# Kernel tuning notes

Measured on AMD Instinct MI355X. Metric: run time of the kernel, lower is better.

The kernel has to match this reference:

```python
import jax, jax.numpy as jnp
import numpy as np

H = 512  # hidden_size


def setup_inputs() -> dict:
    key = jax.random.key(0)
    k1, k2, k3, k4, k5 = jax.random.split(key, 5)
    B, S = 32, 2048
    hidden = jax.random.normal(k1, (1, B, H), dtype=jnp.float32)
    encoder_outputs = jax.random.normal(k2, (B, S, 2 * H), dtype=jnp.float32)
    # nn.Linear(3H, H): weight [H, 3H], store transposed [3H, H] for x @ W
    scale_a = 1.0 / np.sqrt(3 * H)
    Wa = jax.random.uniform(k3, (3 * H, H), jnp.float32, -scale_a, scale_a)
    ba = jax.random.uniform(k4, (H,), jnp.float32, -scale_a, scale_a)
    # nn.Linear(H, 1, bias=False): weight [1, H] -> store as [H]
    scale_v = 1.0 / np.sqrt(H)
    v = jax.random.uniform(k5, (H,), jnp.float32, -scale_v, scale_v)
    return {"hidden": hidden, "encoder_outputs": encoder_outputs,
            "Wa": Wa, "ba": ba, "v": v}


def reference(hidden, encoder_outputs, Wa, ba, v):
    # hidden: [1, B, H] -> [B, H]; encoder_outputs: [B, S, 2H]
    h = jnp.squeeze(hidden, axis=0)                      # [B, H]
    # Split concat-linear into two projections (same math as cat + matmul):
    Wh, We = Wa[:H], Wa[H:]                              # [H, H], [2H, H]
    # energy: [B, S, H] = tanh(h Wh + enc We + b), h broadcast over S
    energy = jnp.tanh(h @ Wh + jnp.einsum('bse,eh->bsh', encoder_outputs, We)[..., :, :] + ba) if False else \
             jnp.tanh((h @ Wh)[:, None, :] + jnp.einsum('bse,eh->bsh', encoder_outputs, We) + ba)
    scores = jnp.einsum('bsh,h->bs', energy, v)          # [B, S]
    attention_weights = jax.nn.softmax(scores, axis=1)   # [B, S]
    context = jnp.einsum('bs,bse->be', attention_weights, encoder_outputs)  # [B, 2H]
    return context, attention_weights
```

## Files before the change

kernel.cpp:

```cpp
#include <hip/hip_runtime.h>

typedef unsigned short ushort_t;
typedef __attribute__((ext_vector_type(8))) short bf16x8;
typedef __attribute__((ext_vector_type(4))) float f32x4;

#define H 512
#define E 1024
#define S 2048
#define B 32

__device__ __forceinline__ ushort_t f2bf(float f) {
    unsigned u = __float_as_uint(f);
    unsigned r = (u + 0x7FFFu + ((u >> 16) & 1u)) >> 16;
    return (ushort_t)r;
}

__device__ __forceinline__ uint4 pack8(float4 x, float4 y) {
    uint4 u;
    u.x = (unsigned)f2bf(x.x) | ((unsigned)f2bf(x.y) << 16);
    u.y = (unsigned)f2bf(x.z) | ((unsigned)f2bf(x.w) << 16);
    u.z = (unsigned)f2bf(y.x) | ((unsigned)f2bf(y.y) << 16);
    u.w = (unsigned)f2bf(y.z) | ((unsigned)f2bf(y.w) << 16);
    return u;
}

__global__ void prep_hb(const float* __restrict__ hidden, const float* __restrict__ Wa,
                        const float* __restrict__ ba, float* __restrict__ hb) {
    int b = blockIdx.x, kc = blockIdx.y, tid = threadIdx.x;
    const float* hp = hidden + b * H + kc * 64;
    float a0 = 0.f, a1 = 0.f;
    #pragma unroll 8
    for (int k = 0; k < 64; ++k) {
        float hv = hp[k];
        a0 += hv * Wa[(size_t)(kc * 64 + k) * H + tid];
        a1 += hv * Wa[(size_t)(kc * 64 + k) * H + tid + 256];
    }
    if (kc == 0) { a0 += ba[tid]; a1 += ba[tid + 256]; }
    atomicAdd(&hb[b * H + tid], a0);
    atomicAdd(&hb[b * H + tid + 256], a1);
}

__global__ void prep_wef(const float* __restrict__ Wa, ushort_t* __restrict__ wef) {
    int g = blockIdx.x * 256 + threadIdx.x;
    int kt = g >> 11, nt = (g >> 6) & 31, l = g & 63;
    int kbase = kt * 32 + ((l >> 4) << 3);
    int n = nt * 16 + (l & 15);
    #pragma unroll
    for (int j = 0; j < 8; ++j)
        wef[(size_t)g * 8 + j] = f2bf(Wa[(size_t)(H + kbase + j) * H + n]);
}

__launch_bounds__(256, 2)
__global__ void score_kernel(const float* __restrict__ enc, const ushort_t* __restrict__ wef,
                             const float* __restrict__ hb, const float* __restrict__ v,
                             float* __restrict__ scores) {
    int b = blockIdx.y;
    int s0 = blockIdx.x * 64;
    int tid = threadIdx.x;
    int wave = tid >> 6, lane = tid & 63;
    int q = lane >> 4, nl = lane & 15;

    __shared__ ushort_t Bs[2][32 * 64 * 8];
    __shared__ ushort_t As[2][64 * 40];
    __shared__ float sred[4][64];

    f32x4 acc[4][8] = {};

    int arow = tid >> 2, acol = (tid & 3) * 8;
    const float* asrc = enc + ((size_t)b * S + s0 + arow) * E + acol;

    const ushort_t* bsrc = wef + (size_t)wave * 4096 + (size_t)lane * 8;

    float4 areg[2][2];
    areg[0][0] = *(const float4*)(asrc);
    areg[0][1] = *(const float4*)(asrc + 4);
    areg[1][0] = *(const float4*)(asrc + 32);
    areg[1][1] = *(const float4*)(asrc + 36);

    #pragma unroll
    for (int j = 0; j < 8; ++j)
        __builtin_amdgcn_global_load_lds(
            (const __attribute__((address_space(1))) unsigned*)(bsrc + j * 512),
            (__attribute__((address_space(3))) unsigned*)(&Bs[0][wave * 4096 + j * 512]),
            16, 0, 0);

    *(uint4*)&As[0][arow * 40 + acol] = pack8(areg[0][0], areg[0][1]);
    __syncthreads();

    for (int kt = 0; kt < 32; ++kt) {
        int cur = kt & 1;
        ushort_t* Ac = &As[cur][0];
        ushort_t* Bc = &Bs[cur][0];

        if (kt < 31) {
            const ushort_t* bs = bsrc + (size_t)(kt + 1) * 16384;
            #pragma unroll
            for (int j = 0; j < 8; ++j)
                __builtin_amdgcn_global_load_lds(
                    (const __attribute__((address_space(1))) unsigned*)(bs + j * 512),
                    (__attribute__((address_space(3))) unsigned*)(&Bs[1 - cur][wave * 4096 + j * 512]),
                    16, 0, 0);
            *(uint4*)&As[1 - cur][arow * 40 + acol] =
                pack8(areg[1 - cur][0], areg[1 - cur][1]);
        }
        if (kt < 30) {
            areg[cur][0] = *(const float4*)(asrc + (size_t)(kt + 2) * 32);
            areg[cur][1] = *(const float4*)(asrc + (size_t)(kt + 2) * 32 + 4);
        }

        bf16x8 afr[4];
        #pragma unroll
        for (int mt = 0; mt < 4; ++mt)
            afr[mt] = *(const bf16x8*)&Ac[(mt * 16 + nl) * 40 + q * 8];
        #pragma unroll
        for (int ntl = 0; ntl < 8; ++ntl) {
            bf16x8 bfr = *(const bf16x8*)&Bc[((wave * 8 + ntl) * 64 + lane) * 8];
            #pragma unroll
            for (int mt = 0; mt < 4; ++mt)
                acc[mt][ntl] = __builtin_amdgcn_mfma_f32_16x16x32_bf16(
                    afr[mt], bfr, acc[mt][ntl], 0, 0, 0);
        }
        __syncthreads();
    }

    float p[16];
    #pragma unroll
    for (int i = 0; i < 16; ++i) p[i] = 0.f;
    #pragma unroll
    for (int ntl = 0; ntl < 8; ++ntl) {
        int n = wave * 128 + ntl * 16 + nl;
        float hv = hb[b * H + n];
        float vv = v[n];
        #pragma unroll
        for (int mt = 0; mt < 4; ++mt)
            #pragma unroll
            for (int r = 0; r < 4; ++r)
                p[mt * 4 + r] += vv * tanhf(acc[mt][ntl][r] + hv);
    }
    #pragma unroll
    for (int off = 1; off < 16; off <<= 1) {
        #pragma unroll
        for (int i = 0; i < 16; ++i) p[i] += __shfl_xor(p[i], off, 64);
    }
    if (nl == 0) {
        #pragma unroll
        for (int mt = 0; mt < 4; ++mt)
            #pragma unroll
            for (int r = 0; r < 4; ++r)
                sred[wave][mt * 16 + q * 4 + r] = p[mt * 4 + r];
    }
    __syncthreads();
    if (tid < 64) {
        float s = sred[0][tid] + sred[1][tid] + sred[2][tid] + sred[3][tid];
        scores[(size_t)b * S + s0 + tid] = s;
    }
}

__global__ void softmax_kernel(const float* __restrict__ scores, float* __restrict__ out) {
    int b = blockIdx.x, tid = threadIdx.x;
    const float* row = scores + (size_t)b * S;
    float loc[8];
    float mx = -3.4e38f;
    #pragma unroll
    for (int i = 0; i < 8; ++i) { loc[i] = row[tid + i * 256]; mx = fmaxf(mx, loc[i]); }
    #pragma unroll
    for (int off = 32; off > 0; off >>= 1) mx = fmaxf(mx, __shfl_xor(mx, off, 64));
    __shared__ float wm[4], wsm[4];
    if ((tid & 63) == 0) wm[tid >> 6] = mx;
    __syncthreads();
    mx = fmaxf(fmaxf(wm[0], wm[1]), fmaxf(wm[2], wm[3]));
    float sum = 0.f;
    #pragma unroll
    for (int i = 0; i < 8; ++i) { loc[i] = __expf(loc[i] - mx); sum += loc[i]; }
    #pragma unroll
    for (int off = 32; off > 0; off >>= 1) sum += __shfl_xor(sum, off, 64);
    if ((tid & 63) == 0) wsm[tid >> 6] = sum;
    __syncthreads();
    sum = wsm[0] + wsm[1] + wsm[2] + wsm[3];
    float inv = 1.f / sum;
    #pragma unroll
    for (int i = 0; i < 8; ++i) out[B * E + (size_t)b * S + tid + i * 256] = loc[i] * inv;
    #pragma unroll
    for (int i = 0; i < 4; ++i) out[(size_t)b * E + tid + i * 256] = 0.f;
}

__global__ void context_kernel(const float* __restrict__ enc, const float* __restrict__ w_attn,
                               float* __restrict__ out_ctx) {
    int sc = blockIdx.x, b = blockIdx.y;
    int e = threadIdx.x * 4;
    const float* w  = w_attn + (size_t)b * S + sc * 128;
    const float* ep = enc + ((size_t)b * S + sc * 128) * E + e;
    float a0 = 0.f, a1 = 0.f, a2 = 0.f, a3 = 0.f;
    #pragma unroll 4
    for (int s = 0; s < 128; ++s) {
        float ws = w[s];
        float4 x = *(const float4*)(ep + (size_t)s * E);
        a0 += ws * x.x; a1 += ws * x.y; a2 += ws * x.z; a3 += ws * x.w;
    }
    float* dst = &out_ctx[(size_t)b * E + e];
    atomicAdd(dst + 0, a0);
    atomicAdd(dst + 1, a1);
    atomicAdd(dst + 2, a2);
    atomicAdd(dst + 3, a3);
}

extern "C" void kernel_launch(void* const* d_in, const int* in_sizes, int n_in,
                              void* d_out, int out_size, void* d_ws, size_t ws_size,
                              hipStream_t stream) {
    const float* hidden = (const float*)d_in[0];
    const float* enc    = (const float*)d_in[1];
    const float* Wa     = (const float*)d_in[2];
    const float* ba     = (const float*)d_in[3];
    const float* v      = (const float*)d_in[4];
    float* out = (float*)d_out;

    char* ws = (char*)d_ws;
    ushort_t* wef = (ushort_t*)ws;
    float* hb     = (float*)(ws + (1 << 20));
    float* scores = (float*)(ws + (1 << 20) + (1 << 16));

    hipMemsetAsync(hb, 0, B * H * sizeof(float), stream);
    prep_hb<<<dim3(B, 8), 256, 0, stream>>>(hidden, Wa, ba, hb);
    prep_wef<<<256, 256, 0, stream>>>(Wa, wef);
    score_kernel<<<dim3(S / 64, B), 256, 0, stream>>>(enc, wef, hb, v, scores);
    softmax_kernel<<<B, 256, 0, stream>>>(scores, out);
    context_kernel<<<dim3(16, B), 256, 0, stream>>>(enc, out + B * E, out);
}
```

Measured before the change: 557.4 us.

## Stage fp32 encoder tiles directly into LDS and convert to bf16 at fragment load

```diff
diff --git a/kernel.cpp b/kernel.cpp
--- a/kernel.cpp
+++ b/kernel.cpp
@@ -15,13 +15,10 @@
     return (ushort_t)r;
 }
 
-__device__ __forceinline__ uint4 pack8(float4 x, float4 y) {
-    uint4 u;
-    u.x = (unsigned)f2bf(x.x) | ((unsigned)f2bf(x.y) << 16);
-    u.y = (unsigned)f2bf(x.z) | ((unsigned)f2bf(x.w) << 16);
-    u.z = (unsigned)f2bf(y.x) | ((unsigned)f2bf(y.y) << 16);
-    u.w = (unsigned)f2bf(y.z) | ((unsigned)f2bf(y.w) << 16);
-    return u;
+__device__ __forceinline__ unsigned pkbf(float x, float y) {
+    unsigned u0 = __float_as_uint(x) + 0x8000u;
+    unsigned u1 = __float_as_uint(y) + 0x8000u;
+    return __builtin_amdgcn_perm(u1, u0, 0x07060302u);
 }
 
 __global__ void prep_hb(const float* __restrict__ hidden, const float* __restrict__ Wa,
@@ -60,68 +57,71 @@
     int wave = tid >> 6, lane = tid & 63;
     int q = lane >> 4, nl = lane & 15;
 
-    __shared__ ushort_t Bs[2][32 * 64 * 8];
-    __shared__ ushort_t As[2][64 * 40];
-    __shared__ float sred[4][64];
+    __shared__ char arena[81920];
+    float* sred = (float*)arena;
 
     f32x4 acc[4][8] = {};
 
-    int arow = tid >> 2, acol = (tid & 3) * 8;
-    const float* asrc = enc + ((size_t)b * S + s0 + arow) * E + acol;
-
-    const ushort_t* bsrc = wef + (size_t)wave * 4096 + (size_t)lane * 8;
-
-    float4 areg[2][2];
-    areg[0][0] = *(const float4*)(asrc);
-    areg[0][1] = *(const float4*)(asrc + 4);
-    areg[1][0] = *(const float4*)(asrc + 32);
-    areg[1][1] = *(const float4*)(asrc + 36);
-
-    #pragma unroll
-    for (int j = 0; j < 8; ++j)
-        __builtin_amdgcn_global_load_lds(
-            (const __attribute__((address_space(1))) unsigned*)(bsrc + j * 512),
-            (__attribute__((address_space(3))) unsigned*)(&Bs[0][wave * 4096 + j * 512]),
-            16, 0, 0);
-
-    *(uint4*)&As[0][arow * 40 + acol] = pack8(areg[0][0], areg[0][1]);
-    __syncthreads();
-
-    for (int kt = 0; kt < 32; ++kt) {
-        int cur = kt & 1;
-        ushort_t* Ac = &As[cur][0];
-        ushort_t* Bc = &Bs[cur][0];
-
-        if (kt < 31) {
-            const ushort_t* bs = bsrc + (size_t)(kt + 1) * 16384;
-            #pragma unroll
-            for (int j = 0; j < 8; ++j)
-                __builtin_amdgcn_global_load_lds(
-                    (const __attribute__((address_space(1))) unsigned*)(bs + j * 512),
-                    (__attribute__((address_space(3))) unsigned*)(&Bs[1 - cur][wave * 4096 + j * 512]),
-                    16, 0, 0);
-            *(uint4*)&As[1 - cur][arow * 40 + acol] =
-                pack8(areg[1 - cur][0], areg[1 - cur][1]);
-        }
-        if (kt < 30) {
-            areg[cur][0] = *(const float4*)(asrc + (size_t)(kt + 2) * 32);
-            areg[cur][1] = *(const float4*)(asrc + (size_t)(kt + 2) * 32 + 4);
-        }
-
-        bf16x8 afr[4];
-        #pragma unroll
-        for (int mt = 0; mt < 4; ++mt)
-            afr[mt] = *(const bf16x8*)&Ac[(mt * 16 + nl) * 40 + q * 8];
-        #pragma unroll
-        for (int ntl = 0; ntl < 8; ++ntl) {
-            bf16x8 bfr = *(const bf16x8*)&Bc[((wave * 8 + ntl) * 64 + lane) * 8];
-            #pragma unroll
-            for (int mt = 0; mt < 4; ++mt)
-                acc[mt][ntl] = __builtin_amdgcn_mfma_f32_16x16x32_bf16(
-                    afr[mt], bfr, acc[mt][ntl], 0, 0, 0);
-        }
+    const char* bsrc = (const char*)wef + wave * 8192 + lane * 16;
+    int r0 = wave * 16 + (lane >> 3);
+    int c4 = ((lane & 7) ^ (lane >> 3)) * 4;
+    const float* asrc0 = enc + ((size_t)b * S + s0 + r0) * E + c4;
+    const float* asrc1 = asrc0 + 8 * E;
+
+#define STAGE(KT, D)                                                                     \
+    {                                                                                    \
+        const char* bp = bsrc + (size_t)(KT) * 32768;                                    \
+        char* bl = arena + (D) * 32768 + wave * 8192;                                    \
+        _Pragma("unroll")                                                                \
+        for (int j = 0; j < 8; ++j)                                                      \
+            __builtin_amdgcn_global_load_lds(                                            \
+                (const __attribute__((address_space(1))) unsigned*)(bp + j * 1024),      \
+                (__attribute__((address_space(3))) unsigned*)(bl + j * 1024), 16, 0, 0); \
+        char* al = arena + 65536 + (D) * 8192 + wave * 2048;                             \
+        __builtin_amdgcn_global_load_lds(                                                \
+            (const __attribute__((address_space(1))) unsigned*)(asrc0 + (KT) * 32),      \
+            (__attribute__((address_space(3))) unsigned*)(al), 16, 0, 0);                \
+        __builtin_amdgcn_global_load_lds(                                                \
+            (const __attribute__((address_space(1))) unsigned*)(asrc1 + (KT) * 32),      \
+            (__attribute__((address_space(3))) unsigned*)(al + 1024), 16, 0, 0);         \
+    }
+
+#define COMPUTE(CUR)                                                                     \
+    {                                                                                    \
+        const ushort_t* Bc = (const ushort_t*)(arena + (CUR) * 32768);                   \
+        const float*    Ac = (const float*)(arena + 65536 + (CUR) * 8192);               \
+        bf16x8 afr[4];                                                                   \
+        _Pragma("unroll")                                                                \
+        for (int mt = 0; mt < 4; ++mt) {                                                 \
+            int r = mt * 16 + nl;                                                        \
+            int sa = r * 8 + ((2 * q) ^ (nl & 7));                                       \
+            int sb = r * 8 + ((2 * q + 1) ^ (nl & 7));                                   \
+            float4 f0 = *(const float4*)(Ac + sa * 4);                                   \
+            float4 f1 = *(const float4*)(Ac + sb * 4);                                   \
+            uint4 u;                                                                     \
+            u.x = pkbf(f0.x, f0.y); u.y = pkbf(f0.z, f0.w);                              \
+            u.z = pkbf(f1.x, f1.y); u.w = pkbf(f1.z, f1.w);                              \
+            afr[mt] = *(bf16x8*)&u;                                                      \
+        }                                                                                \
+        _Pragma("unroll")                                                                \
+        for (int ntl = 0; ntl < 8; ++ntl) {                                              \
+            bf16x8 bfr = *(const bf16x8*)&Bc[((wave * 8 + ntl) * 64 + lane) * 8];        \
+            _Pragma("unroll")                                                            \
+            for (int mt = 0; mt < 4; ++mt)                                               \
+                acc[mt][ntl] = __builtin_amdgcn_mfma_f32_16x16x32_bf16(                  \
+                    afr[mt], bfr, acc[mt][ntl], 0, 0, 0);                                \
+        }                                                                                \
+    }
+
+    STAGE(0, 0);
+    __syncthreads();
+    for (int kt = 0; kt < 31; ++kt) {
+        STAGE(kt + 1, (kt + 1) & 1);
+        COMPUTE(kt & 1);
         __syncthreads();
     }
+    COMPUTE(1);
+    __syncthreads();
 
     float p[16];
     #pragma unroll
@@ -147,13 +147,15 @@
         for (int mt = 0; mt < 4; ++mt)
             #pragma unroll
             for (int r = 0; r < 4; ++r)
-                sred[wave][mt * 16 + q * 4 + r] = p[mt * 4 + r];
+                sred[wave * 64 + mt * 16 + q * 4 + r] = p[mt * 4 + r];
     }
     __syncthreads();
     if (tid < 64) {
-        float s = sred[0][tid] + sred[1][tid] + sred[2][tid] + sred[3][tid];
+        float s = sred[tid] + sred[64 + tid] + sred[128 + tid] + sred[192 + tid];
         scores[(size_t)b * S + s0 + tid] = s;
     }
+#undef STAGE
+#undef COMPUTE
 }
 
 __global__ void softmax_kernel(const float* __restrict__ scores, float* __restrict__ out) {
@@ -188,11 +190,11 @@
                                float* __restrict__ out_ctx) {
     int sc = blockIdx.x, b = blockIdx.y;
     int e = threadIdx.x * 4;
-    const float* w  = w_attn + (size_t)b * S + sc * 128;
-    const float* ep = enc + ((size_t)b * S + sc * 128) * E + e;
+    const float* w  = w_attn + (size_t)b * S + sc * 64;
+    const float* ep = enc + ((size_t)b * S + sc * 64) * E + e;
     float a0 = 0.f, a1 = 0.f, a2 = 0.f, a3 = 0.f;
-    #pragma unroll 4
-    for (int s = 0; s < 128; ++s) {
+    #pragma unroll 8
+    for (int s = 0; s < 64; ++s) {
         float ws = w[s];
         float4 x = *(const float4*)(ep + (size_t)s * E);
         a0 += ws * x.x; a1 += ws * x.y; a2 += ws * x.z; a3 += ws * x.w;
@@ -224,5 +226,5 @@
     prep_wef<<<256, 256, 0, stream>>>(Wa, wef);
     score_kernel<<<dim3(S / 64, B), 256, 0, stream>>>(enc, wef, hb, v, scores);
     softmax_kernel<<<B, 256, 0, stream>>>(scores, out);
-    context_kernel<<<dim3(16, B), 256, 0, stream>>>(enc, out + B * E, out);
-}
+    context_kernel<<<dim3(32, B), 256, 0, stream>>>(enc, out + B * E, out);
+}
```

Result: faster. 499.6 us (-10.4%).
